# Optimization experiments

Hardware: AMD Instinct MI355X
Metric: run time of the kernel (lower is better)

Reference implementation:

```python
import jax, jax.numpy as jnp
import numpy as np

VIS_DIM = 768
LBL_DIM = 128
HID = 256
VIS_W = 0.4
LBL_W = 0.6
TEMP = 1.0
EPS = 1e-12  # torch F.normalize default eps


def setup_inputs() -> dict:
    key = jax.random.key(0)
    ks = jax.random.split(key, 8)
    B, N = 32, 4096
    visual_feats = jax.random.normal(ks[0], (B, N, VIS_DIM), dtype=jnp.float32)
    label_context = jax.random.normal(ks[1], (B, LBL_DIM), dtype=jnp.float32)
    visual_mask = jnp.ones((B, N), dtype=bool)
    # scorer MLP params (stored [in, out] for x @ W)
    W1 = jax.random.normal(ks[2], (VIS_DIM, HID), dtype=jnp.float32) / np.sqrt(VIS_DIM)
    b1 = jnp.zeros((HID,), dtype=jnp.float32)
    W2 = jax.random.normal(ks[3], (HID, 1), dtype=jnp.float32) / np.sqrt(HID)
    b2 = jnp.zeros((1,), dtype=jnp.float32)
    # label -> visual projection
    Wp = jax.random.normal(ks[4], (LBL_DIM, VIS_DIM), dtype=jnp.float32) / np.sqrt(LBL_DIM)
    bp = jnp.zeros((VIS_DIM,), dtype=jnp.float32)
    return {
        "visual_feats": visual_feats,
        "label_context": label_context,
        "W1": W1, "b1": b1, "W2": W2, "b2": b2, "Wp": Wp, "bp": bp,
        "visual_mask": visual_mask,
        "k": 192,
    }


def _l2norm(x):
    n = jnp.linalg.norm(x, axis=-1, keepdims=True)
    return x / jnp.maximum(n, EPS)


def reference(visual_feats, label_context, W1, b1, W2, b2, Wp, bp, visual_mask, k):
    B, N, D = visual_feats.shape
    # scoring MLP: [B,N,D] -> [B,N]
    h = jnp.maximum(jnp.einsum('bnd,dh->bnh', visual_feats, W1) + b1, 0.0)
    visual_scores = (jnp.einsum('bnh,ho->bno', h, W2) + b2)[..., 0]
    # label projection [B,D] then cosine similarity against each patch
    label_proj = label_context @ Wp + bp              # [B, D]
    vis_n = _l2norm(visual_feats)                     # [B, N, D]
    lbl_n = _l2norm(label_proj)[:, None, :]           # [B, 1, D]
    label_scores = jnp.sum(vis_n * lbl_n, axis=-1)    # [B, N]
    combined = (VIS_W * visual_scores + LBL_W * label_scores) / TEMP
    combined = jnp.where(visual_mask, combined, -jnp.inf)
    k = min(int(k), N)
    topk_scores, topk_indices = jax.lax.top_k(combined, k)   # [B, k]
    selected_feats = jnp.take_along_axis(visual_feats, topk_indices[..., None], axis=1)
    return selected_feats, topk_indices
```

## Files before the change

### kernel.cpp

```cpp
#include <hip/hip_runtime.h>
#include <hip/hip_bf16.h>

#define B_   32
#define N_   4096
#define D_   768
#define HID_ 256

#define SX 64.0f
#define SW 1024.0f
#define INV_S (1.0f / 65536.0f)

typedef unsigned long long ull;
typedef _Float16 half8 __attribute__((ext_vector_type(8)));
typedef _Float16 half4 __attribute__((ext_vector_type(4)));
typedef float f32x16 __attribute__((ext_vector_type(16)));

__global__ __launch_bounds__(256) void wsplit_kernel(
    const float* __restrict__ W1, _Float16* __restrict__ whi,
    _Float16* __restrict__ wlo) {
  int c = blockIdx.x;
  int h = threadIdx.x;
  half8 vh, vl;
#pragma unroll
  for (int j = 0; j < 8; ++j) {
    float w = W1[(size_t)(c * 8 + j) * 256 + h] * SW;
    _Float16 hi = (_Float16)w;
    vh[j] = hi;
    vl[j] = (_Float16)(w - (float)hi);
  }
  *(half8*)&whi[((size_t)c * 256 + h) * 8] = vh;
  *(half8*)&wlo[((size_t)c * 256 + h) * 8] = vl;
}

__global__ __launch_bounds__(256) void proj_norm_kernel(
    const float* __restrict__ lc, const float* __restrict__ Wp,
    const float* __restrict__ bp, float* __restrict__ lbl_n) {
  int b = blockIdx.x;
  int t = threadIdx.x;
  __shared__ float s_lc[128];
  __shared__ float s_out[768];
  __shared__ float s_red[4];

  if (t < 128) s_lc[t] = lc[b * 128 + t];
  __syncthreads();

  float sumsq = 0.f;
  for (int d = t; d < D_; d += 256) {
    float acc = bp[d];
    for (int k = 0; k < 128; ++k) acc += s_lc[k] * Wp[k * D_ + d];
    s_out[d] = acc;
    sumsq += acc * acc;
  }
  for (int off = 32; off >= 1; off >>= 1) sumsq += __shfl_xor(sumsq, off);
  if ((t & 63) == 0) s_red[t >> 6] = sumsq;
  __syncthreads();
  float tot = s_red[0] + s_red[1] + s_red[2] + s_red[3];
  float inv = 1.f / fmaxf(sqrtf(tot), 1e-12f);
  for (int d = t; d < D_; d += 256) lbl_n[b * D_ + d] = s_out[d] * inv;
}

__global__ __launch_bounds__(256, 3) void score3_kernel(
    const float* __restrict__ X, const _Float16* __restrict__ Whi,
    const _Float16* __restrict__ Wlo, const float* __restrict__ b1,
    const float* __restrict__ W2, const float* __restrict__ b2,
    const float* __restrict__ lbl_n, float* __restrict__ scores) {
  __shared__ __align__(16) _Float16 sW[2][2][2][256][8];
  __shared__ __align__(16) _Float16 sB[2][2][2][64][8];
  __shared__ __align__(16) float sLbl[768];
  __shared__ float sB1[256], sW2[256];
  __shared__ float sVs[2][64];
  __shared__ float sLsc[64];

  const int t  = threadIdx.x;
  const int w  = t >> 6;
  const int l  = t & 63;
  const int l5 = l >> 5;
  const int ln = l & 31;
  const int pg = w & 1;
  const int hh = w >> 1;
  const int pb = blockIdx.x * 64;
  const int batch = pb >> 12;

  for (int i = t; i < D_; i += 256) sLbl[i] = lbl_n[batch * D_ + i];
  sB1[t] = b1[t];
  sW2[t] = W2[t];

  const int srow = t >> 2;
  const int sk   = t & 3;
  const float* xrow = X + (size_t)(pb + srow) * D_;

  f32x16 acc[4];
#pragma unroll
  for (int mt = 0; mt < 4; ++mt)
#pragma unroll
    for (int r = 0; r < 16; ++r) acc[mt][r] = 0.f;

  const float4* gWh = (const float4*)Whi;
  const float4* gWl = (const float4*)Wlo;

  float sq = 0.f, dt = 0.f;

  float4 wh0 = gWh[t],        wh1 = gWh[256 + t];
  float4 wl0 = gWl[t],        wl1 = gWl[256 + t];
  float4 xr  = *(const float4*)&xrow[sk * 4];

  __syncthreads();

  {
    float4 lv = *(const float4*)&sLbl[sk * 4];
    half4 h_, l_;
#pragma unroll
    for (int j = 0; j < 4; ++j) {
      float xv = (&xr.x)[j];
      sq += xv * xv;
      dt += xv * (&lv.x)[j];
      float xs = xv * SX;
      _Float16 hi = (_Float16)xs;
      h_[j] = hi;
      l_[j] = (_Float16)(xs - (float)hi);
    }
    *(half4*)&sB[0][0][sk >> 1][srow][(sk & 1) * 4] = h_;
    *(half4*)&sB[0][1][sk >> 1][srow][(sk & 1) * 4] = l_;
    float4* dh = (float4*)&sW[0][0][0][0][0];
    float4* dl = (float4*)&sW[0][1][0][0][0];
    dh[t] = wh0; dh[256 + t] = wh1;
    dl[t] = wl0; dl[256 + t] = wl1;
  }
  __syncthreads();

  for (int s = 0; s < 48; ++s) {
    const int cur = s & 1;
    if (s < 47) {
      const int sn = s + 1;
      wh0 = gWh[sn * 512 + t];       wh1 = gWh[sn * 512 + 256 + t];
      wl0 = gWl[sn * 512 + t];       wl1 = gWl[sn * 512 + 256 + t];
      xr  = *(const float4*)&xrow[sn * 16 + sk * 4];
    }

    half8 bh = *(const half8*)&sB[cur][0][l5][pg * 32 + ln][0];
    half8 bl = *(const half8*)&sB[cur][1][l5][pg * 32 + ln][0];
#pragma unroll
    for (int mt = 0; mt < 4; ++mt) {
      half8 ah = *(const half8*)&sW[cur][0][l5][hh * 128 + mt * 32 + ln][0];
      half8 al = *(const half8*)&sW[cur][1][l5][hh * 128 + mt * 32 + ln][0];
      acc[mt] = __builtin_amdgcn_mfma_f32_32x32x16_f16(ah, bh, acc[mt], 0, 0, 0);
      acc[mt] = __builtin_amdgcn_mfma_f32_32x32x16_f16(ah, bl, acc[mt], 0, 0, 0);
      acc[mt] = __builtin_amdgcn_mfma_f32_32x32x16_f16(al, bh, acc[mt], 0, 0, 0);
    }

    if (s < 47) {
      const int nb = cur ^ 1;
      float4 lv = *(const float4*)&sLbl[(s + 1) * 16 + sk * 4];
      half4 h_, l_;
#pragma unroll
      for (int j = 0; j < 4; ++j) {
        float xv = (&xr.x)[j];
        sq += xv * xv;
        dt += xv * (&lv.x)[j];
        float xs = xv * SX;
        _Float16 hi = (_Float16)xs;
        h_[j] = hi;
        l_[j] = (_Float16)(xs - (float)hi);
      }
      *(half4*)&sB[nb][0][sk >> 1][srow][(sk & 1) * 4] = h_;
      *(half4*)&sB[nb][1][sk >> 1][srow][(sk & 1) * 4] = l_;
      float4* dh = (float4*)&sW[nb][0][0][0][0];
      float4* dl = (float4*)&sW[nb][1][0][0][0];
      dh[t] = wh0; dh[256 + t] = wh1;
      dl[t] = wl0; dl[256 + t] = wl1;
    }
    __syncthreads();
  }

  sq += __shfl_xor(sq, 1); dt += __shfl_xor(dt, 1);
  sq += __shfl_xor(sq, 2); dt += __shfl_xor(dt, 2);
  if ((l & 3) == 0) sLsc[srow] = dt / fmaxf(sqrtf(sq), 1e-12f);

  float vs = 0.f;
#pragma unroll
  for (int mt = 0; mt < 4; ++mt) {
#pragma unroll
    for (int rq = 0; rq < 4; ++rq) {
      const int hb = hh * 128 + mt * 32 + rq * 8 + l5 * 4;
      const float4 b1v = *(const float4*)&sB1[hb];
      const float4 w2v = *(const float4*)&sW2[hb];
      float hv0 = acc[mt][rq * 4 + 0] * INV_S + b1v.x;
      float hv1 = acc[mt][rq * 4 + 1] * INV_S + b1v.y;
      float hv2 = acc[mt][rq * 4 + 2] * INV_S + b1v.z;
      float hv3 = acc[mt][rq * 4 + 3] * INV_S + b1v.w;
      vs += fmaxf(hv0, 0.f) * w2v.x;
      vs += fmaxf(hv1, 0.f) * w2v.y;
      vs += fmaxf(hv2, 0.f) * w2v.z;
      vs += fmaxf(hv3, 0.f) * w2v.w;
    }
  }
  vs += __shfl_xor(vs, 32);
  if (l < 32) sVs[hh][pg * 32 + l] = vs;
  __syncthreads();

  if (w < 2 && l < 32) {
    int p = w * 32 + l;
    float vst = sVs[0][p] + sVs[1][p] + b2[0];
    scores[pb + p] = 0.4f * vst + 0.6f * sLsc[p];
  }
}

__global__ __launch_bounds__(256) void topk2_kernel(
    const float* __restrict__ scores, int* __restrict__ out_idx, int K) {
  int b = blockIdx.x;
  int t = threadIdx.x;
  __shared__ ull swm[4];

  ull keys[16];
#pragma unroll
  for (int j = 0; j < 16; ++j) {
    int i = (j << 8) + t;
    float s = scores[(b << 12) + i];
    unsigned u = __float_as_uint(s);
    u = (u & 0x80000000u) ? ~u : (u | 0x80000000u);
    keys[j] = ((ull)u << 32) | (unsigned)(4095 - i);
  }
  ull cur = 0;
#pragma unroll
  for (int j = 0; j < 16; ++j) cur = keys[j] > cur ? keys[j] : cur;

  for (int sel = 0; sel < K; ++sel) {
    ull wb = cur;
#pragma unroll
    for (int off = 1; off < 64; off <<= 1) {
      ull o = __shfl_xor(wb, off);
      wb = o > wb ? o : wb;
    }
    if ((t & 63) == 0) swm[t >> 6] = wb;
    __syncthreads();
    ull m0 = swm[0] > swm[1] ? swm[0] : swm[1];
    ull m1 = swm[2] > swm[3] ? swm[2] : swm[3];
    ull best = m0 > m1 ? m0 : m1;
    if (t == 0) out_idx[b * K + sel] = 4095 - (int)(unsigned)(best & 0xFFFFFFFFull);
    if (cur == best) {
      cur = 0;
#pragma unroll
      for (int j = 0; j < 16; ++j)
        cur = (keys[j] < best && keys[j] > cur) ? keys[j] : cur;
    }
    __syncthreads();
  }
}

__global__ __launch_bounds__(192) void gather_kernel(
    const float* __restrict__ feats, const int* __restrict__ idx,
    float* __restrict__ out_feats, float* __restrict__ out_idx_f, int K) {
  int i = blockIdx.x;
  int b = blockIdx.y;
  int id = idx[b * K + i];
  const float4* src = (const float4*)&feats[((size_t)b * N_ + id) * D_];
  float4* dst = (float4*)&out_feats[((size_t)b * K + i) * D_];
  dst[threadIdx.x] = src[threadIdx.x];
  if (threadIdx.x == 0) out_idx_f[b * K + i] = (float)id;
}

extern "C" void kernel_launch(void* const* d_in, const int* in_sizes, int n_in,
                              void* d_out, int out_size, void* d_ws, size_t ws_size,
                              hipStream_t stream) {
  const float* feats = (const float*)d_in[0];
  const float* lc    = (const float*)d_in[1];
  const float* W1    = (const float*)d_in[2];
  const float* b1    = (const float*)d_in[3];
  const float* W2    = (const float*)d_in[4];
  const float* b2    = (const float*)d_in[5];
  const float* Wp    = (const float*)d_in[6];
  const float* bp    = (const float*)d_in[7];
  int K = out_size / (B_ * (D_ + 1));

  float* ws_f    = (float*)d_ws;
  float* lbl_n   = ws_f;
  float* scoresv = ws_f + B_ * D_;
  int*   topidx  = (int*)(ws_f + B_ * D_ + B_ * N_);
  size_t off = (size_t)B_ * D_ + (size_t)B_ * N_ + B_ * 256;
  off = (off + 3) & ~(size_t)3;
  _Float16* whi = (_Float16*)(ws_f + off);
  _Float16* wlo = whi + (size_t)96 * 256 * 8;

  float* out_f     = (float*)d_out;
  float* out_idx_f = out_f + (size_t)B_ * K * D_;

  wsplit_kernel<<<96, 256, 0, stream>>>(W1, whi, wlo);
  proj_norm_kernel<<<B_, 256, 0, stream>>>(lc, Wp, bp, lbl_n);
  score3_kernel<<<(B_ * N_) / 64, 256, 0, stream>>>(feats, whi, wlo, b1, W2, b2,
                                                    lbl_n, scoresv);
  topk2_kernel<<<B_, 256, 0, stream>>>(scoresv, topidx, K);
  gather_kernel<<<dim3(K, B_), 192, 0, stream>>>(feats, topidx, out_f, out_idx_f, K);
}
```

Baseline: 399.2 us.

## Keep W1 fragments in registers and repartition waves by hidden slice

The scoring kernel stops staging W1 hi/lo tiles through shared memory. Each wave now loads its own 64-hidden-column slice of W1 directly from global memory into registers, prefetched one step ahead. The wave-to-tile mapping changes from (point-group, hidden-half) to hidden-quarter across all 64 points, so each wave computes 2x2 MFMA tiles and the partial MLP scores are reduced over four waves. This removes shared-memory writes and reads of W1 and shrinks LDS use, in exchange for more global/L2 traffic for W1 per block and higher register pressure.

Measured after the change: 350.2 us. 1.14x faster.

```diff
diff --git a/kernel.cpp b/kernel.cpp
--- a/kernel.cpp
+++ b/kernel.cpp
@@ -59,16 +59,15 @@
   for (int d = t; d < D_; d += 256) lbl_n[b * D_ + d] = s_out[d] * inv;
 }
 
-__global__ __launch_bounds__(256, 3) void score3_kernel(
+__global__ __launch_bounds__(256, 3) void score4_kernel(
     const float* __restrict__ X, const _Float16* __restrict__ Whi,
     const _Float16* __restrict__ Wlo, const float* __restrict__ b1,
     const float* __restrict__ W2, const float* __restrict__ b2,
     const float* __restrict__ lbl_n, float* __restrict__ scores) {
-  __shared__ __align__(16) _Float16 sW[2][2][2][256][8];
   __shared__ __align__(16) _Float16 sB[2][2][2][64][8];
   __shared__ __align__(16) float sLbl[768];
   __shared__ float sB1[256], sW2[256];
-  __shared__ float sVs[2][64];
+  __shared__ float sVs[4][64];
   __shared__ float sLsc[64];
 
   const int t  = threadIdx.x;
@@ -76,8 +75,6 @@
   const int l  = t & 63;
   const int l5 = l >> 5;
   const int ln = l & 31;
-  const int pg = w & 1;
-  const int hh = w >> 1;
   const int pb = blockIdx.x * 64;
   const int batch = pb >> 12;
 
@@ -89,20 +86,23 @@
   const int sk   = t & 3;
   const float* xrow = X + (size_t)(pb + srow) * D_;
 
-  f32x16 acc[4];
-#pragma unroll
-  for (int mt = 0; mt < 4; ++mt)
-#pragma unroll
-    for (int r = 0; r < 16; ++r) acc[mt][r] = 0.f;
-
-  const float4* gWh = (const float4*)Whi;
-  const float4* gWl = (const float4*)Wlo;
+  f32x16 acc[2][2];
+#pragma unroll
+  for (int pt = 0; pt < 2; ++pt)
+#pragma unroll
+    for (int mt = 0; mt < 2; ++mt)
+#pragma unroll
+      for (int r = 0; r < 16; ++r) acc[pt][mt][r] = 0.f;
+
+  const half8* gWh = (const half8*)Whi;
+  const half8* gWl = (const half8*)Wlo;
+  const int hidb = w * 64 + ln;
 
   float sq = 0.f, dt = 0.f;
 
-  float4 wh0 = gWh[t],        wh1 = gWh[256 + t];
-  float4 wl0 = gWl[t],        wl1 = gWl[256 + t];
-  float4 xr  = *(const float4*)&xrow[sk * 4];
+  half8 ah0 = gWh[l5 * 256 + hidb],      ah1 = gWh[l5 * 256 + hidb + 32];
+  half8 al0 = gWl[l5 * 256 + hidb],      al1 = gWl[l5 * 256 + hidb + 32];
+  float4 xr = *(const float4*)&xrow[sk * 4];
 
   __syncthreads();
 
@@ -121,32 +121,39 @@
     }
     *(half4*)&sB[0][0][sk >> 1][srow][(sk & 1) * 4] = h_;
     *(half4*)&sB[0][1][sk >> 1][srow][(sk & 1) * 4] = l_;
-    float4* dh = (float4*)&sW[0][0][0][0][0];
-    float4* dl = (float4*)&sW[0][1][0][0][0];
-    dh[t] = wh0; dh[256 + t] = wh1;
-    dl[t] = wl0; dl[256 + t] = wl1;
   }
   __syncthreads();
 
   for (int s = 0; s < 48; ++s) {
     const int cur = s & 1;
+    half8 ph0, ph1, pl0, pl1;
+    float4 nxr;
     if (s < 47) {
-      const int sn = s + 1;
-      wh0 = gWh[sn * 512 + t];       wh1 = gWh[sn * 512 + 256 + t];
-      wl0 = gWl[sn * 512 + t];       wl1 = gWl[sn * 512 + 256 + t];
-      xr  = *(const float4*)&xrow[sn * 16 + sk * 4];
-    }
-
-    half8 bh = *(const half8*)&sB[cur][0][l5][pg * 32 + ln][0];
-    half8 bl = *(const half8*)&sB[cur][1][l5][pg * 32 + ln][0];
-#pragma unroll
-    for (int mt = 0; mt < 4; ++mt) {
-      half8 ah = *(const half8*)&sW[cur][0][l5][hh * 128 + mt * 32 + ln][0];
-      half8 al = *(const half8*)&sW[cur][1][l5][hh * 128 + mt * 32 + ln][0];
-      acc[mt] = __builtin_amdgcn_mfma_f32_32x32x16_f16(ah, bh, acc[mt], 0, 0, 0);
-      acc[mt] = __builtin_amdgcn_mfma_f32_32x32x16_f16(ah, bl, acc[mt], 0, 0, 0);
-      acc[mt] = __builtin_amdgcn_mfma_f32_32x32x16_f16(al, bh, acc[mt], 0, 0, 0);
-    }
+      const int c = (s + 1) * 2 + l5;
+      ph0 = gWh[c * 256 + hidb];
+      ph1 = gWh[c * 256 + hidb + 32];
+      pl0 = gWl[c * 256 + hidb];
+      pl1 = gWl[c * 256 + hidb + 32];
+      nxr = *(const float4*)&xrow[(s + 1) * 16 + sk * 4];
+    }
+
+    half8 bh0 = *(const half8*)&sB[cur][0][l5][ln][0];
+    half8 bl0 = *(const half8*)&sB[cur][1][l5][ln][0];
+    half8 bh1 = *(const half8*)&sB[cur][0][l5][32 + ln][0];
+    half8 bl1 = *(const half8*)&sB[cur][1][l5][32 + ln][0];
+
+    acc[0][0] = __builtin_amdgcn_mfma_f32_32x32x16_f16(ah0, bh0, acc[0][0], 0, 0, 0);
+    acc[0][1] = __builtin_amdgcn_mfma_f32_32x32x16_f16(ah1, bh0, acc[0][1], 0, 0, 0);
+    acc[1][0] = __builtin_amdgcn_mfma_f32_32x32x16_f16(ah0, bh1, acc[1][0], 0, 0, 0);
+    acc[1][1] = __builtin_amdgcn_mfma_f32_32x32x16_f16(ah1, bh1, acc[1][1], 0, 0, 0);
+    acc[0][0] = __builtin_amdgcn_mfma_f32_32x32x16_f16(ah0, bl0, acc[0][0], 0, 0, 0);
+    acc[0][1] = __builtin_amdgcn_mfma_f32_32x32x16_f16(ah1, bl0, acc[0][1], 0, 0, 0);
+    acc[1][0] = __builtin_amdgcn_mfma_f32_32x32x16_f16(ah0, bl1, acc[1][0], 0, 0, 0);
+    acc[1][1] = __builtin_amdgcn_mfma_f32_32x32x16_f16(ah1, bl1, acc[1][1], 0, 0, 0);
+    acc[0][0] = __builtin_amdgcn_mfma_f32_32x32x16_f16(al0, bh0, acc[0][0], 0, 0, 0);
+    acc[0][1] = __builtin_amdgcn_mfma_f32_32x32x16_f16(al1, bh0, acc[0][1], 0, 0, 0);
+    acc[1][0] = __builtin_amdgcn_mfma_f32_32x32x16_f16(al0, bh1, acc[1][0], 0, 0, 0);
+    acc[1][1] = __builtin_amdgcn_mfma_f32_32x32x16_f16(al1, bh1, acc[1][1], 0, 0, 0);
 
     if (s < 47) {
       const int nb = cur ^ 1;
@@ -154,7 +161,7 @@
       half4 h_, l_;
 #pragma unroll
       for (int j = 0; j < 4; ++j) {
-        float xv = (&xr.x)[j];
+        float xv = (&nxr.x)[j];
         sq += xv * xv;
         dt += xv * (&lv.x)[j];
         float xs = xv * SX;
@@ -164,10 +171,7 @@
       }
       *(half4*)&sB[nb][0][sk >> 1][srow][(sk & 1) * 4] = h_;
       *(half4*)&sB[nb][1][sk >> 1][srow][(sk & 1) * 4] = l_;
-      float4* dh = (float4*)&sW[nb][0][0][0][0];
-      float4* dl = (float4*)&sW[nb][1][0][0][0];
-      dh[t] = wh0; dh[256 + t] = wh1;
-      dl[t] = wl0; dl[256 + t] = wl1;
+      ah0 = ph0; ah1 = ph1; al0 = pl0; al1 = pl1;
     }
     __syncthreads();
   }
@@ -176,32 +180,34 @@
   sq += __shfl_xor(sq, 2); dt += __shfl_xor(dt, 2);
   if ((l & 3) == 0) sLsc[srow] = dt / fmaxf(sqrtf(sq), 1e-12f);
 
-  float vs = 0.f;
-#pragma unroll
-  for (int mt = 0; mt < 4; ++mt) {
+  float vs0 = 0.f, vs1 = 0.f;
+#pragma unroll
+  for (int mt = 0; mt < 2; ++mt) {
 #pragma unroll
     for (int rq = 0; rq < 4; ++rq) {
-      const int hb = hh * 128 + mt * 32 + rq * 8 + l5 * 4;
+      const int hb = w * 64 + mt * 32 + rq * 8 + l5 * 4;
       const float4 b1v = *(const float4*)&sB1[hb];
       const float4 w2v = *(const float4*)&sW2[hb];
-      float hv0 = acc[mt][rq * 4 + 0] * INV_S + b1v.x;
-      float hv1 = acc[mt][rq * 4 + 1] * INV_S + b1v.y;
-      float hv2 = acc[mt][rq * 4 + 2] * INV_S + b1v.z;
-      float hv3 = acc[mt][rq * 4 + 3] * INV_S + b1v.w;
-      vs += fmaxf(hv0, 0.f) * w2v.x;
-      vs += fmaxf(hv1, 0.f) * w2v.y;
-      vs += fmaxf(hv2, 0.f) * w2v.z;
-      vs += fmaxf(hv3, 0.f) * w2v.w;
-    }
-  }
-  vs += __shfl_xor(vs, 32);
-  if (l < 32) sVs[hh][pg * 32 + l] = vs;
-  __syncthreads();
-
-  if (w < 2 && l < 32) {
-    int p = w * 32 + l;
-    float vst = sVs[0][p] + sVs[1][p] + b2[0];
-    scores[pb + p] = 0.4f * vst + 0.6f * sLsc[p];
+#pragma unroll
+      for (int j = 0; j < 4; ++j) {
+        float h0 = acc[0][mt][rq * 4 + j] * INV_S + (&b1v.x)[j];
+        float h1 = acc[1][mt][rq * 4 + j] * INV_S + (&b1v.x)[j];
+        vs0 += fmaxf(h0, 0.f) * (&w2v.x)[j];
+        vs1 += fmaxf(h1, 0.f) * (&w2v.x)[j];
+      }
+    }
+  }
+  vs0 += __shfl_xor(vs0, 32);
+  vs1 += __shfl_xor(vs1, 32);
+  if (l < 32) {
+    sVs[w][l]      = vs0;
+    sVs[w][32 + l] = vs1;
+  }
+  __syncthreads();
+
+  if (t < 64) {
+    float vst = sVs[0][t] + sVs[1][t] + sVs[2][t] + sVs[3][t] + b2[0];
+    scores[pb + t] = 0.4f * vst + 0.6f * sLsc[t];
   }
 }
 
@@ -286,7 +292,7 @@
 
   wsplit_kernel<<<96, 256, 0, stream>>>(W1, whi, wlo);
   proj_norm_kernel<<<B_, 256, 0, stream>>>(lc, Wp, bp, lbl_n);
-  score3_kernel<<<(B_ * N_) / 64, 256, 0, stream>>>(feats, whi, wlo, b1, W2, b2,
+  score4_kernel<<<(B_ * N_) / 64, 256, 0, stream>>>(feats, whi, wlo, b1, W2, b2,
                                                     lbl_n, scoresv);
   topk2_kernel<<<B_, 256, 0, stream>>>(scoresv, topidx, K);
   gather_kernel<<<dim3(K, B_), 192, 0, stream>>>(feats, topidx, out_f, out_idx_f, K);
```

## Enlarge score kernel tile to 256 patches with 512 threads and deeper X prefetch

Applied to the files above, without the earlier changes.

The scoring GEMM kernel now processes 256 patches per block with 8 waves, each wave computing a 128x64 output tile (4x2 MFMA tiles) instead of 128x32. This amortizes the W1 hi/lo shared-memory traffic over four times more rows, cutting the redundant global reads of the split weights. It also adds a two-stage-ahead register prefetch of X and uses explicit lgkmcnt barriers. The trade-off is a single-buffered W tile, which needs two barriers per stage, and higher register pressure from eight accumulator tiles.

Result: faster. 362.8 us (-9.1%).

```diff
diff --git a/kernel.cpp b/kernel.cpp
--- a/kernel.cpp
+++ b/kernel.cpp
@@ -12,8 +12,12 @@
 
 typedef unsigned long long ull;
 typedef _Float16 half8 __attribute__((ext_vector_type(8)));
-typedef _Float16 half4 __attribute__((ext_vector_type(4)));
 typedef float f32x16 __attribute__((ext_vector_type(16)));
+
+#define LGKM0_BARRIER() do { \
+    asm volatile("s_waitcnt lgkmcnt(0)" ::: "memory"); \
+    __builtin_amdgcn_s_barrier(); \
+  } while (0)
 
 __global__ __launch_bounds__(256) void wsplit_kernel(
     const float* __restrict__ W1, _Float16* __restrict__ whi,
@@ -59,124 +63,162 @@
   for (int d = t; d < D_; d += 256) lbl_n[b * D_ + d] = s_out[d] * inv;
 }
 
-__global__ __launch_bounds__(256, 3) void score3_kernel(
+__global__ __launch_bounds__(512, 2) void score5_kernel(
     const float* __restrict__ X, const _Float16* __restrict__ Whi,
     const _Float16* __restrict__ Wlo, const float* __restrict__ b1,
     const float* __restrict__ W2, const float* __restrict__ b2,
     const float* __restrict__ lbl_n, float* __restrict__ scores) {
-  __shared__ __align__(16) _Float16 sW[2][2][2][256][8];
-  __shared__ __align__(16) _Float16 sB[2][2][2][64][8];
+  __shared__ __align__(16) _Float16 sW[2][2][256][8];
+  __shared__ __align__(16) _Float16 sB[2][2][2][256][8];
   __shared__ __align__(16) float sLbl[768];
   __shared__ float sB1[256], sW2[256];
-  __shared__ float sVs[2][64];
-  __shared__ float sLsc[64];
+  __shared__ float sVs[2][256];
+  __shared__ float sLsc[256];
 
   const int t  = threadIdx.x;
   const int w  = t >> 6;
   const int l  = t & 63;
   const int l5 = l >> 5;
   const int ln = l & 31;
-  const int pg = w & 1;
-  const int hh = w >> 1;
-  const int pb = blockIdx.x * 64;
+  const int hh = w >> 2;
+  const int pg = w & 3;
+  const int pb = blockIdx.x * 256;
   const int batch = pb >> 12;
 
-  for (int i = t; i < D_; i += 256) sLbl[i] = lbl_n[batch * D_ + i];
-  sB1[t] = b1[t];
-  sW2[t] = W2[t];
-
-  const int srow = t >> 2;
-  const int sk   = t & 3;
-  const float* xrow = X + (size_t)(pb + srow) * D_;
-
-  f32x16 acc[4];
-#pragma unroll
-  for (int mt = 0; mt < 4; ++mt)
-#pragma unroll
-    for (int r = 0; r < 16; ++r) acc[mt][r] = 0.f;
+  for (int i = t; i < D_; i += 512) sLbl[i] = lbl_n[batch * D_ + i];
+  if (t < 256) { sB1[t] = b1[t]; sW2[t] = W2[t]; }
+
+  const int r  = t >> 1;
+  const int h2 = t & 1;
+  const float* xrow = X + (size_t)(pb + r) * D_ + h2 * 8;
 
   const float4* gWh = (const float4*)Whi;
   const float4* gWl = (const float4*)Wlo;
 
+  f32x16 acc[4][2];
+#pragma unroll
+  for (int mt = 0; mt < 4; ++mt)
+#pragma unroll
+    for (int bt = 0; bt < 2; ++bt)
+#pragma unroll
+      for (int q = 0; q < 16; ++q) acc[mt][bt][q] = 0.f;
+
   float sq = 0.f, dt = 0.f;
 
-  float4 wh0 = gWh[t],        wh1 = gWh[256 + t];
-  float4 wl0 = gWl[t],        wl1 = gWl[256 + t];
-  float4 xr  = *(const float4*)&xrow[sk * 4];
-
+  float4 xa0 = *(const float4*)(xrow + 0);
+  float4 xa1 = *(const float4*)(xrow + 4);
+  float4 whr = gWh[t];
+  float4 wlr = gWl[t];
   __syncthreads();
 
   {
-    float4 lv = *(const float4*)&sLbl[sk * 4];
-    half4 h_, l_;
-#pragma unroll
-    for (int j = 0; j < 4; ++j) {
-      float xv = (&xr.x)[j];
+    half8 bh, bl;
+#pragma unroll
+    for (int j = 0; j < 8; ++j) {
+      float xv = (j < 4) ? (&xa0.x)[j] : (&xa1.x)[j - 4];
+      float lv = sLbl[h2 * 8 + j];
       sq += xv * xv;
-      dt += xv * (&lv.x)[j];
+      dt += xv * lv;
       float xs = xv * SX;
       _Float16 hi = (_Float16)xs;
-      h_[j] = hi;
-      l_[j] = (_Float16)(xs - (float)hi);
+      bh[j] = hi;
+      bl[j] = (_Float16)(xs - (float)hi);
     }
-    *(half4*)&sB[0][0][sk >> 1][srow][(sk & 1) * 4] = h_;
-    *(half4*)&sB[0][1][sk >> 1][srow][(sk & 1) * 4] = l_;
-    float4* dh = (float4*)&sW[0][0][0][0][0];
-    float4* dl = (float4*)&sW[0][1][0][0][0];
-    dh[t] = wh0; dh[256 + t] = wh1;
-    dl[t] = wl0; dl[256 + t] = wl1;
-  }
-  __syncthreads();
-
-  for (int s = 0; s < 48; ++s) {
-    const int cur = s & 1;
-    if (s < 47) {
-      const int sn = s + 1;
-      wh0 = gWh[sn * 512 + t];       wh1 = gWh[sn * 512 + 256 + t];
-      wl0 = gWl[sn * 512 + t];       wl1 = gWl[sn * 512 + 256 + t];
-      xr  = *(const float4*)&xrow[sn * 16 + sk * 4];
-    }
-
-    half8 bh = *(const half8*)&sB[cur][0][l5][pg * 32 + ln][0];
-    half8 bl = *(const half8*)&sB[cur][1][l5][pg * 32 + ln][0];
-#pragma unroll
-    for (int mt = 0; mt < 4; ++mt) {
-      half8 ah = *(const half8*)&sW[cur][0][l5][hh * 128 + mt * 32 + ln][0];
-      half8 al = *(const half8*)&sW[cur][1][l5][hh * 128 + mt * 32 + ln][0];
-      acc[mt] = __builtin_amdgcn_mfma_f32_32x32x16_f16(ah, bh, acc[mt], 0, 0, 0);
-      acc[mt] = __builtin_amdgcn_mfma_f32_32x32x16_f16(ah, bl, acc[mt], 0, 0, 0);
-      acc[mt] = __builtin_amdgcn_mfma_f32_32x32x16_f16(al, bh, acc[mt], 0, 0, 0);
-    }
-
-    if (s < 47) {
-      const int nb = cur ^ 1;
-      float4 lv = *(const float4*)&sLbl[(s + 1) * 16 + sk * 4];
-      half4 h_, l_;
-#pragma unroll
-      for (int j = 0; j < 4; ++j) {
-        float xv = (&xr.x)[j];
-        sq += xv * xv;
-        dt += xv * (&lv.x)[j];
-        float xs = xv * SX;
-        _Float16 hi = (_Float16)xs;
-        h_[j] = hi;
-        l_[j] = (_Float16)(xs - (float)hi);
-      }
-      *(half4*)&sB[nb][0][sk >> 1][srow][(sk & 1) * 4] = h_;
-      *(half4*)&sB[nb][1][sk >> 1][srow][(sk & 1) * 4] = l_;
-      float4* dh = (float4*)&sW[nb][0][0][0][0];
-      float4* dl = (float4*)&sW[nb][1][0][0][0];
-      dh[t] = wh0; dh[256 + t] = wh1;
-      dl[t] = wl0; dl[256 + t] = wl1;
-    }
-    __syncthreads();
-  }
-
-  sq += __shfl_xor(sq, 1); dt += __shfl_xor(dt, 1);
-  sq += __shfl_xor(sq, 2); dt += __shfl_xor(dt, 2);
-  if ((l & 3) == 0) sLsc[srow] = dt / fmaxf(sqrtf(sq), 1e-12f);
-
-  float vs = 0.f;
+    *(half8*)&sB[0][0][h2][r][0] = bh;
+    *(half8*)&sB[0][1][h2][r][0] = bl;
+    ((float4*)&sW[0][0][0][0])[t] = whr;
+    ((float4*)&sW[1][0][0][0])[t] = wlr;
+  }
+  float4 xb0 = *(const float4*)(xrow + 16);
+  float4 xb1 = *(const float4*)(xrow + 20);
+  LGKM0_BARRIER();
+
+  const int ahid = hh * 128 + ln;
+  const int bpat = pg * 64 + ln;
+
+#define STAGE_BODY(S, XW0, XW1, XL0, XL1)                                      \
+  {                                                                            \
+    const int c = (S) & 1;                                                     \
+                                                 \
+    {                                                                          \
+      const int s2 = ((S) + 2 > 47) ? 47 : (S) + 2;                            \
+      XL0 = *(const float4*)(xrow + s2 * 16);                                  \
+      XL1 = *(const float4*)(xrow + s2 * 16 + 4);                              \
+    }                                                                          \
+                                                             \
+    {                                                                          \
+      const int s1 = ((S) + 1 > 47) ? 47 : (S) + 1;                            \
+      whr = gWh[s1 * 512 + t];                                                 \
+      wlr = gWl[s1 * 512 + t];                                                 \
+    }                                                                          \
+                                                \
+    {                                                                          \
+      half8 ah[4], al[4], bh[2], bl[2];                                        \
+      _Pragma("unroll")                                                        \
+      for (int mt = 0; mt < 4; ++mt) {                                         \
+        ah[mt] = *(const half8*)&sW[0][l5][ahid + mt * 32][0];                 \
+        al[mt] = *(const half8*)&sW[1][l5][ahid + mt * 32][0];                 \
+      }                                                                        \
+      _Pragma("unroll")                                                        \
+      for (int bt = 0; bt < 2; ++bt) {                                         \
+        bh[bt] = *(const half8*)&sB[c][0][l5][bpat + bt * 32][0];              \
+        bl[bt] = *(const half8*)&sB[c][1][l5][bpat + bt * 32][0];              \
+      }                                                                        \
+      _Pragma("unroll")                                                        \
+      for (int mt = 0; mt < 4; ++mt)                                           \
+        _Pragma("unroll")                                                      \
+        for (int bt = 0; bt < 2; ++bt)                                         \
+          acc[mt][bt] = __builtin_amdgcn_mfma_f32_32x32x16_f16(                \
+              ah[mt], bh[bt], acc[mt][bt], 0, 0, 0);                           \
+      _Pragma("unroll")                                                        \
+      for (int mt = 0; mt < 4; ++mt)                                           \
+        _Pragma("unroll")                                                      \
+        for (int bt = 0; bt < 2; ++bt)                                         \
+          acc[mt][bt] = __builtin_amdgcn_mfma_f32_32x32x16_f16(                \
+              ah[mt], bl[bt], acc[mt][bt], 0, 0, 0);                           \
+      _Pragma("unroll")                                                        \
+      for (int mt = 0; mt < 4; ++mt)                                           \
+        _Pragma("unroll")                                                      \
+        for (int bt = 0; bt < 2; ++bt)                                         \
+          acc[mt][bt] = __builtin_amdgcn_mfma_f32_32x32x16_f16(                \
+              al[mt], bh[bt], acc[mt][bt], 0, 0, 0);                           \
+    }                                                                          \
+                                      \
+    half8 nbh, nbl;                                                            \
+    if ((S) < 47) {                                                            \
+      _Pragma("unroll")                                                        \
+      for (int j = 0; j < 8; ++j) {                                            \
+        float xv = (j < 4) ? (&XW0.x)[j] : (&XW1.x)[j - 4];                    \
+        float lv = sLbl[((S) + 1) * 16 + h2 * 8 + j];                          \
+        sq += xv * xv;                                                         \
+        dt += xv * lv;                                                         \
+        float xs = xv * SX;                                                    \
+        _Float16 hi = (_Float16)xs;                                            \
+        nbh[j] = hi;                                                           \
+        nbl[j] = (_Float16)(xs - (float)hi);                                   \
+      }                                                                        \
+    }                                                                          \
+    LGKM0_BARRIER();                           \
+    if ((S) < 47) {                                                            \
+      ((float4*)&sW[0][0][0][0])[t] = whr;                                     \
+      ((float4*)&sW[1][0][0][0])[t] = wlr;                                     \
+      *(half8*)&sB[c ^ 1][0][h2][r][0] = nbh;                                  \
+      *(half8*)&sB[c ^ 1][1][h2][r][0] = nbl;                                  \
+    }                                                                          \
+    LGKM0_BARRIER();                                       \
+  }
+
+  for (int s = 0; s < 48; s += 2) {
+    STAGE_BODY(s,     xb0, xb1, xa0, xa1)
+    STAGE_BODY(s + 1, xa0, xa1, xb0, xb1)
+  }
+#undef STAGE_BODY
+
+  sq += __shfl_xor(sq, 1);
+  dt += __shfl_xor(dt, 1);
+  if (h2 == 0) sLsc[r] = dt / fmaxf(sqrtf(sq), 1e-12f);
+
+  float vsb[2] = {0.f, 0.f};
 #pragma unroll
   for (int mt = 0; mt < 4; ++mt) {
 #pragma unroll
@@ -184,24 +226,26 @@
       const int hb = hh * 128 + mt * 32 + rq * 8 + l5 * 4;
       const float4 b1v = *(const float4*)&sB1[hb];
       const float4 w2v = *(const float4*)&sW2[hb];
-      float hv0 = acc[mt][rq * 4 + 0] * INV_S + b1v.x;
-      float hv1 = acc[mt][rq * 4 + 1] * INV_S + b1v.y;
-      float hv2 = acc[mt][rq * 4 + 2] * INV_S + b1v.z;
-      float hv3 = acc[mt][rq * 4 + 3] * INV_S + b1v.w;
-      vs += fmaxf(hv0, 0.f) * w2v.x;
-      vs += fmaxf(hv1, 0.f) * w2v.y;
-      vs += fmaxf(hv2, 0.f) * w2v.z;
-      vs += fmaxf(hv3, 0.f) * w2v.w;
+#pragma unroll
+      for (int j = 0; j < 4; ++j) {
+        float h0 = acc[mt][0][rq * 4 + j] * INV_S + (&b1v.x)[j];
+        float h1 = acc[mt][1][rq * 4 + j] * INV_S + (&b1v.x)[j];
+        vsb[0] += fmaxf(h0, 0.f) * (&w2v.x)[j];
+        vsb[1] += fmaxf(h1, 0.f) * (&w2v.x)[j];
+      }
     }
   }
-  vs += __shfl_xor(vs, 32);
-  if (l < 32) sVs[hh][pg * 32 + l] = vs;
+  vsb[0] += __shfl_xor(vsb[0], 32);
+  vsb[1] += __shfl_xor(vsb[1], 32);
+  if (l < 32) {
+    sVs[hh][pg * 64 + l]      = vsb[0];
+    sVs[hh][pg * 64 + 32 + l] = vsb[1];
+  }
   __syncthreads();
 
-  if (w < 2 && l < 32) {
-    int p = w * 32 + l;
-    float vst = sVs[0][p] + sVs[1][p] + b2[0];
-    scores[pb + p] = 0.4f * vst + 0.6f * sLsc[p];
+  if (t < 256) {
+    float vst = sVs[0][t] + sVs[1][t] + b2[0];
+    scores[pb + t] = 0.4f * vst + 0.6f * sLsc[t];
   }
 }
 
@@ -286,8 +330,8 @@
 
   wsplit_kernel<<<96, 256, 0, stream>>>(W1, whi, wlo);
   proj_norm_kernel<<<B_, 256, 0, stream>>>(lc, Wp, bp, lbl_n);
-  score3_kernel<<<(B_ * N_) / 64, 256, 0, stream>>>(feats, whi, wlo, b1, W2, b2,
-                                                    lbl_n, scoresv);
+  score5_kernel<<<(B_ * N_) / 256, 512, 0, stream>>>(feats, whi, wlo, b1, W2, b2,
+                                                     lbl_n, scoresv);
   topk2_kernel<<<B_, 256, 0, stream>>>(scoresv, topidx, K);
   gather_kernel<<<dim3(K, B_), 192, 0, stream>>>(feats, topidx, out_f, out_idx_f, K);
 }
```
